# Optimization experiments

Measured on AMD Instinct MI355X. Metric: run time of the kernel, lower is better.

Reference implementation:

```python
import jax, jax.numpy as jnp
import numpy as np

B, N, E, H = 2, 2048, 1024, 16
D = E // H  # head_dim = 64


def setup_inputs() -> dict:
    key = jax.random.key(0)
    ks = jax.random.split(key, 8)
    s = 1.0 / np.sqrt(D)
    return {
        "query": jax.random.normal(ks[0], (B, N, E), jnp.float32),
        "key": jax.random.normal(ks[1], (B, N, E), jnp.float32),
        "value": jax.random.normal(ks[2], (B, N, E), jnp.float32),
        "mask": jax.random.randint(ks[3], (B, N), 0, 2, jnp.int32),
        # per-head Linear weights, torch layout (out_features, in_features) stacked over heads
        "Wq": jax.random.uniform(ks[4], (H, D, D), jnp.float32, -s, s),
        "Wk": jax.random.uniform(ks[5], (H, D, D), jnp.float32, -s, s),
        "Wv": jax.random.uniform(ks[6], (H, D, D), jnp.float32, -s, s),
        "Wo": jax.random.uniform(ks[7], (E, E), jnp.float32, -1.0 / np.sqrt(E), 1.0 / np.sqrt(E)),
    }


def reference(query, key, value, mask, Wq, Wk, Wv, Wo):
    b, n, e = query.shape
    h, d, _ = Wq.shape
    q = query.reshape(b, n, h, d)
    k = key.reshape(b, n, h, d)
    v = value.reshape(b, n, h, d)
    # per-head Linear (no bias): x @ W[i].T, batched over heads
    qh = jnp.einsum('bnhd,hed->bnhe', q, Wq)
    kh = jnp.einsum('bnhd,hed->bnhe', k, Wk)
    vh = jnp.einsum('bnhd,hed->bnhe', v, Wv)
    # NOTE: original scales by sqrt(embed_size), not sqrt(head_dim)
    scores = jnp.einsum('bqhd,bkhd->bhqk', qh, kh) / (e ** 0.5)
    # NOTE: mask is unsqueezed on the KEY axis position in torch (dim=2),
    # so it masks entire QUERY rows, broadcasting over keys.
    scores = jnp.where(mask[:, None, :, None] == 0, jnp.float32(-1e28), scores)
    probs = jax.nn.softmax(scores, axis=-1)
    attn = jnp.einsum('bhqk,bkhd->bqhd', probs, vh).reshape(b, n, e)
    return attn @ Wo.T
```

## Files before the change

### kernel.cpp

```cpp
#include <hip/hip_runtime.h>
#include <hip/hip_bf16.h>

#define B_ 2
#define N_ 2048
#define E_ 1024
#define H_ 16
#define D_ 64
#define BH_ (B_ * H_)

typedef __attribute__((ext_vector_type(4))) float f32x4;
typedef __attribute__((ext_vector_type(8))) short bf16x8;
typedef __attribute__((ext_vector_type(4))) short s16x4;
typedef __attribute__((ext_vector_type(4))) int i32x4;
typedef __attribute__((ext_vector_type(2))) int i32x2;
typedef __attribute__((ext_vector_type(4))) _Float16 f16x4;

#define MFMA(a, b, c) __builtin_amdgcn_mfma_f32_16x16x32_bf16(a, b, c, 0, 0, 0)
#define MFMA16(a, b, c) __builtin_amdgcn_mfma_f32_16x16x16f16(a, b, c, 0, 0, 0)

#define AS1(p) ((const __attribute__((address_space(1))) unsigned int*)(p))
#define AS3(p) ((__attribute__((address_space(3))) unsigned int*)(p))

static __device__ __forceinline__ int pack2bf(float lo, float hi) {
    __hip_bfloat162 t = __float22bfloat162_rn(float2{lo, hi});
    int r;
    __builtin_memcpy(&r, &t, 4);
    return r;
}
static __device__ __forceinline__ bf16x8 cvt8s(const float* __restrict__ p, float sc) {
    f32x4 a = *(const f32x4*)p;
    f32x4 b = *(const f32x4*)(p + 4);
    i32x4 r = {pack2bf(a.x * sc, a.y * sc), pack2bf(a.z * sc, a.w * sc),
               pack2bf(b.x * sc, b.y * sc), pack2bf(b.z * sc, b.w * sc)};
    return __builtin_bit_cast(bf16x8, r);
}
static __device__ __forceinline__ f16x4 pack4f16(f32x4 p) {
    auto lo = __builtin_amdgcn_cvt_pkrtz(p.x, p.y);
    auto hi = __builtin_amdgcn_cvt_pkrtz(p.z, p.w);
    f16x4 r;
    __builtin_memcpy(&r, &lo, 4);
    __builtin_memcpy(((char*)&r) + 4, &hi, 4);
    return r;
}

__global__ __launch_bounds__(256, 2)
void proj_kernel(const float* __restrict__ q, const float* __restrict__ k,
                 const float* __restrict__ v,
                 const float* __restrict__ Wq, const float* __restrict__ Wk,
                 const float* __restrict__ Wv,
                 const int* __restrict__ mask,
                 const float* __restrict__ Wo,
                 unsigned short* __restrict__ qh, unsigned short* __restrict__ kh,
                 unsigned short* __restrict__ vt, unsigned short* __restrict__ wob) {
    const int z = blockIdx.z;
    if (z == 3) {
        int idx = (blockIdx.y * 32 + blockIdx.x) * 256 + threadIdx.x;
        f32x4 w = *(const f32x4*)(Wo + (size_t)idx * 4);
        i32x2 r = {pack2bf(w.x, w.y), pack2bf(w.z, w.w)};
        *(i32x2*)(wob + (size_t)idx * 4) = r;
        return;
    }
    const float* X = (z == 0) ? q : (z == 1) ? k : v;
    const float* W = (z == 0) ? Wq : (z == 1) ? Wk : Wv;
    unsigned short* out = (z == 0) ? qh : (z == 1) ? kh : vt;
    const float wscale = (z == 0) ? (1.44269504f * 0.03125f) : 1.0f;

    const int lane = threadIdx.x & 63;
    const int wave = threadIdx.x >> 6;
    const int l16  = lane & 15;
    const int quad = lane >> 4;
    const int bh = blockIdx.y;
    const int b = bh >> 4, h = bh & 15;
    const int n0 = blockIdx.x * 64;
    const int tok = n0 + wave * 16 + l16;

    const float* xrow = X + ((size_t)(b * N_ + tok)) * E_ + h * 64;
    bf16x8 xf[2];
    xf[0] = cvt8s(xrow + quad * 8, 1.0f);
    xf[1] = cvt8s(xrow + 32 + quad * 8, 1.0f);

    const float* Wh = W + (size_t)h * 64 * 64;
    bf16x8 wf[4][2];
#pragma unroll
    for (int t4 = 0; t4 < 4; ++t4) {
        const float* wrow = Wh + (t4 * 16 + l16) * 64;
        wf[t4][0] = cvt8s(wrow + quad * 8, wscale);
        wf[t4][1] = cvt8s(wrow + 32 + quad * 8, wscale);
    }

    const int mk = (z == 0) ? mask[b * N_ + tok] : 1;

#pragma unroll
    for (int mi = 0; mi < 4; ++mi) {
        f32x4 a = {0.f, 0.f, 0.f, 0.f};
        a = MFMA(wf[mi][0], xf[0], a);
        a = MFMA(wf[mi][1], xf[1], a);
        if (z != 2) {
            i32x2 pk = {pack2bf(a.x, a.y), pack2bf(a.z, a.w)};
            if (!mk) pk = (i32x2){0, 0};
            *(i32x2*)(out + ((size_t)bh * N_ + tok) * 64 + mi * 16 + quad * 4) = pk;
        } else {
#pragma unroll
            for (int r = 0; r < 4; ++r) {
                int dout = mi * 16 + quad * 4 + r;
                _Float16 hv = (_Float16)a[r];
                unsigned short us;
                __builtin_memcpy(&us, &hv, 2);
                out[((size_t)bh * 64 + dout) * N_ + tok] = us;
            }
        }
    }
}

__global__ __launch_bounds__(256)
void cvt_wo_kernel(const float* __restrict__ wo, unsigned short* __restrict__ wob) {
    int idx = blockIdx.x * 256 + threadIdx.x;
    f32x4 v = *(const f32x4*)(wo + (size_t)idx * 4);
    i32x2 r = {pack2bf(v.x, v.y), pack2bf(v.z, v.w)};
    *(i32x2*)(wob + (size_t)idx * 4) = r;
}

__global__ __launch_bounds__(256, 2)
void attn_kernel(const unsigned short* __restrict__ qh,
                 const unsigned short* __restrict__ kh,
                 const unsigned short* __restrict__ vt,
                 unsigned short* __restrict__ attnb) {
    __shared__ short Kb[2][64 * 72];
    __shared__ short Vb[3][64 * 76];

    const int tid  = threadIdx.x;
    const int lane = tid & 63;
    const int wave = tid >> 6;
    const int l16  = lane & 15;
    const int quad = lane >> 4;

    const int flat = blockIdx.y * gridDim.x + blockIdx.x;
    const int qblk = flat >> 5;
    const int rem  = flat & 31;
    const int bh   = ((rem & 7) << 2) | (rem >> 3);
    const int b = bh >> 4, h = bh & 15;
    const int q0 = qblk * 128 + wave * 32;

    const unsigned short* kbase = kh + (size_t)bh * N_ * 64;
    const unsigned short* vbase = vt + (size_t)bh * 64 * N_;

    const int c0i = tid;
    const int c1i = tid + 256;
    const int k0o = (c0i >> 3) * 72 + (c0i & 7) * 8;
    const int k1o = (c1i >> 3) * 72 + (c1i & 7) * 8;
    const int v0o = (c0i >> 3) * 76 + (c0i & 7) * 8;
    const int v1o = (c1i >> 3) * 76 + (c1i & 7) * 8;

    short* kcur  = &Kb[0][0];
    short* knext = &Kb[1][0];
    short* vprev = &Vb[2][0];
    short* vcur  = &Vb[0][0];
    short* vnext = &Vb[1][0];

    bf16x8 qf[2][2];
#pragma unroll
    for (int qi = 0; qi < 2; ++qi) {
        const unsigned short* qrow = qh + ((size_t)bh * N_ + q0 + qi * 16 + l16) * 64;
        qf[qi][0] = *(const bf16x8*)(qrow + quad * 8);
        qf[qi][1] = *(const bf16x8*)(qrow + 32 + quad * 8);
    }

    f32x4 psum[2] = {{0.f, 0.f, 0.f, 0.f}, {0.f, 0.f, 0.f, 0.f}};
    f32x4 o[4][2];
#pragma unroll
    for (int mi = 0; mi < 4; ++mi)
#pragma unroll
        for (int qi = 0; qi < 2; ++qi) o[mi][qi] = (f32x4){0.f, 0.f, 0.f, 0.f};

    f16x4 pf[2][4];

    bf16x8 gK0, gK1, gV0, gV1;
    gK0 = *(const bf16x8*)(kbase + c0i * 8);
    gK1 = *(const bf16x8*)(kbase + c1i * 8);
    gV0 = *(const bf16x8*)(vbase + (size_t)(c0i >> 3) * N_ + (c0i & 7) * 8);
    gV1 = *(const bf16x8*)(vbase + (size_t)(c1i >> 3) * N_ + (c1i & 7) * 8);
    *(bf16x8*)(kcur + k0o) = gK0;
    *(bf16x8*)(kcur + k1o) = gK1;
    *(bf16x8*)(vcur + v0o) = gV0;
    *(bf16x8*)(vcur + v1o) = gV1;
    __syncthreads();

    for (int kt = 0; kt < N_ / 64; ++kt) {
        if (kt + 1 < N_ / 64) {
            const int k0n = (kt + 1) * 64;
            gK0 = *(const bf16x8*)(kbase + (size_t)k0n * 64 + c0i * 8);
            gK1 = *(const bf16x8*)(kbase + (size_t)k0n * 64 + c1i * 8);
            gV0 = *(const bf16x8*)(vbase + (size_t)(c0i >> 3) * N_ + k0n + (c0i & 7) * 8);
            gV1 = *(const bf16x8*)(vbase + (size_t)(c1i >> 3) * N_ + k0n + (c1i & 7) * 8);
        }

        __builtin_amdgcn_s_setprio(1);
        bf16x8 ka[4][2];
#pragma unroll
        for (int t4 = 0; t4 < 4; ++t4) {
            ka[t4][0] = *(const bf16x8*)(kcur + (t4 * 16 + l16) * 72 + quad * 8);
            ka[t4][1] = *(const bf16x8*)(kcur + (t4 * 16 + l16) * 72 + 32 + quad * 8);
        }
        f32x4 s[2][4];
#pragma unroll
        for (int qi = 0; qi < 2; ++qi)
#pragma unroll
            for (int t4 = 0; t4 < 4; ++t4) {
                f32x4 z = {0.f, 0.f, 0.f, 0.f};
                z = MFMA(ka[t4][0], qf[qi][0], z);
                z = MFMA(ka[t4][1], qf[qi][1], z);
                s[qi][t4] = z;
            }

        if (kt > 0) {
#pragma unroll
            for (int mi = 0; mi < 4; ++mi) {
#pragma unroll
                for (int t4 = 0; t4 < 4; ++t4) {
                    f16x4 va = *(const f16x4*)(vprev + (mi * 16 + l16) * 76 +
                                               t4 * 16 + quad * 4);
#pragma unroll
                    for (int qi = 0; qi < 2; ++qi)
                        o[mi][qi] = MFMA16(va, pf[qi][t4], o[mi][qi]);
                }
            }
        }
        __builtin_amdgcn_s_setprio(0);

#pragma unroll
        for (int qi = 0; qi < 2; ++qi) {
#pragma unroll
            for (int t4 = 0; t4 < 4; ++t4) {
                f32x4 p;
#pragma unroll
                for (int r = 0; r < 4; ++r) p[r] = __builtin_amdgcn_exp2f(s[qi][t4][r]);
                psum[qi] += p;
                pf[qi][t4] = pack4f16(p);
            }
        }

        if (kt + 1 < N_ / 64) {
            *(bf16x8*)(knext + k0o) = gK0;
            *(bf16x8*)(knext + k1o) = gK1;
            *(bf16x8*)(vnext + v0o) = gV0;
            *(bf16x8*)(vnext + v1o) = gV1;
            __syncthreads();
        }

        short* t = kcur; kcur = knext; knext = t;
        short* tv = vprev; vprev = vcur; vcur = vnext; vnext = tv;
    }

    __builtin_amdgcn_s_setprio(1);
#pragma unroll
    for (int mi = 0; mi < 4; ++mi) {
#pragma unroll
        for (int t4 = 0; t4 < 4; ++t4) {
            f16x4 va = *(const f16x4*)(vprev + (mi * 16 + l16) * 76 +
                                       t4 * 16 + quad * 4);
#pragma unroll
            for (int qi = 0; qi < 2; ++qi)
                o[mi][qi] = MFMA16(va, pf[qi][t4], o[mi][qi]);
        }
    }
    __builtin_amdgcn_s_setprio(0);

#pragma unroll
    for (int qi = 0; qi < 2; ++qi) {
        float rs = psum[qi].x + psum[qi].y + psum[qi].z + psum[qi].w;
        rs += __shfl_xor(rs, 16);
        rs += __shfl_xor(rs, 32);
        const float inv = 1.0f / rs;
        const int qrow_idx = q0 + qi * 16 + l16;
#pragma unroll
        for (int mi = 0; mi < 4; ++mi) {
            f32x4 ov = o[mi][qi];
            i32x2 pkk = {pack2bf(ov.x * inv, ov.y * inv),
                         pack2bf(ov.z * inv, ov.w * inv)};
            int d0 = mi * 16 + quad * 4;
            *(i32x2*)(attnb + ((size_t)(b * N_ + qrow_idx)) * E_ + h * 64 + d0) = pkk;
        }
    }
}

__global__ __launch_bounds__(512, 1)
void out_gemm_kernel(const unsigned short* __restrict__ A,
                     const unsigned short* __restrict__ Bw,
                     float* __restrict__ out) {
    __shared__ short As[2][128 * 32];
    __shared__ short Bs[2][128 * 32];

    const int tid  = threadIdx.x;
    const int lane = tid & 63;
    const int l16  = lane & 15;
    const int quad = lane >> 4;
    const int wave = tid >> 6;
    const int wm = wave & 1, wn = wave >> 1;

    const int flat = blockIdx.x;
    const int xcd  = flat & 7;
    const int sub  = flat >> 3;
    const int m0 = (xcd * 4 + (sub >> 3)) * 128;
    const int n0 = (sub & 7) * 128;

    const unsigned short* gA = A + (size_t)m0 * E_;
    const unsigned short* gB = Bw + (size_t)n0 * E_;

    f32x4 acc[4][2];
#pragma unroll
    for (int mt = 0; mt < 4; ++mt)
#pragma unroll
        for (int nt = 0; nt < 2; ++nt) acc[mt][nt] = (f32x4){0.f, 0.f, 0.f, 0.f};

    const int cc = tid >> 7, rr = tid & 127;
#define OG_STAGE(buf, k0)                                                        \
    {                                                                            \
        __builtin_amdgcn_global_load_lds(AS1(gA + (size_t)rr * E_ + (k0) + cc * 8), \
                                         AS3(&As[buf][tid * 8]), 16, 0, 0);      \
        __builtin_amdgcn_global_load_lds(AS1(gB + (size_t)rr * E_ + (k0) + cc * 8), \
                                         AS3(&Bs[buf][tid * 8]), 16, 0, 0);      \
    }

    OG_STAGE(0, 0)
    __syncthreads();

    for (int kt = 0; kt < E_ / 32; ++kt) {
        const int cur = kt & 1;
        if (kt + 1 < E_ / 32) OG_STAGE(cur ^ 1, (kt + 1) * 32)

        bf16x8 af[4], bf[2];
#pragma unroll
        for (int mt = 0; mt < 4; ++mt)
            af[mt] = *(const bf16x8*)(&As[cur][(quad * 128 + wm * 64 + mt * 16 + l16) * 8]);
#pragma unroll
        for (int nt = 0; nt < 2; ++nt)
            bf[nt] = *(const bf16x8*)(&Bs[cur][(quad * 128 + wn * 32 + nt * 16 + l16) * 8]);

        __builtin_amdgcn_s_setprio(1);
#pragma unroll
        for (int mt = 0; mt < 4; ++mt)
#pragma unroll
            for (int nt = 0; nt < 2; ++nt)
                acc[mt][nt] = MFMA(af[mt], bf[nt], acc[mt][nt]);
        __builtin_amdgcn_s_setprio(0);

        __syncthreads();
    }

#pragma unroll
    for (int mt = 0; mt < 4; ++mt)
#pragma unroll
        for (int nt = 0; nt < 2; ++nt)
#pragma unroll
            for (int r = 0; r < 4; ++r)
                out[(size_t)(m0 + wm * 64 + mt * 16 + quad * 4 + r) * E_ +
                    n0 + wn * 32 + nt * 16 + l16] = acc[mt][nt][r];
#undef OG_STAGE
}

extern "C" void kernel_launch(void* const* d_in, const int* in_sizes, int n_in,
                              void* d_out, int out_size, void* d_ws, size_t ws_size,
                              hipStream_t stream) {
    const float* q    = (const float*)d_in[0];
    const float* k    = (const float*)d_in[1];
    const float* v    = (const float*)d_in[2];
    const int*   mask = (const int*)d_in[3];
    const float* Wq   = (const float*)d_in[4];
    const float* Wk   = (const float*)d_in[5];
    const float* Wv   = (const float*)d_in[6];
    const float* Wo   = (const float*)d_in[7];
    float* out = (float*)d_out;

    char* ws = (char*)d_ws;
    unsigned short* qh    = (unsigned short*)(ws);
    unsigned short* kh    = (unsigned short*)(ws + (size_t)8 * 1024 * 1024);
    unsigned short* vt    = (unsigned short*)(ws + (size_t)16 * 1024 * 1024);
    unsigned short* attnb = (unsigned short*)(ws + (size_t)24 * 1024 * 1024);

    const bool fused_wo = ws_size >= (size_t)34 * 1024 * 1024;
    unsigned short* wob = fused_wo ? (unsigned short*)(ws + (size_t)32 * 1024 * 1024)
                                   : (unsigned short*)(ws);

    dim3 blk(256);
    proj_kernel<<<dim3(N_ / 64, BH_, fused_wo ? 4 : 3), blk, 0, stream>>>(
        q, k, v, Wq, Wk, Wv, mask, Wo, qh, kh, vt, wob);
    attn_kernel<<<dim3(16, 32), blk, 0, stream>>>(qh, kh, vt, attnb);
    if (!fused_wo)
        cvt_wo_kernel<<<dim3(E_ * E_ / 1024), blk, 0, stream>>>(Wo, wob);
    out_gemm_kernel<<<dim3(256), dim3(512), 0, stream>>>(attnb, wob, out);
}
```

Measured before the change: 197.5 us.

## Load K and V fragments directly from global memory, dropping LDS staging

Removes the shared-memory double/triple buffers and __syncthreads in the attention loop. Each wave now loads its K and V MFMA fragments straight from global (L2/L1) into registers, with K prefetched one tile ahead via ping-pong register arrays and the loop unrolled by two. The goal is to cut LDS traffic and barrier stalls, at the cost of every wave redundantly fetching the same K/V tiles from cache, narrower uncoalesced V loads, and more register pressure. The PV MFMA is no longer software-pipelined one iteration behind.

```diff
diff --git a/kernel.cpp b/kernel.cpp
--- a/kernel.cpp
+++ b/kernel.cpp
@@ -125,9 +125,6 @@
                  const unsigned short* __restrict__ kh,
                  const unsigned short* __restrict__ vt,
                  unsigned short* __restrict__ attnb) {
-    __shared__ short Kb[2][64 * 72];
-    __shared__ short Vb[3][64 * 76];
-
     const int tid  = threadIdx.x;
     const int lane = tid & 63;
     const int wave = tid >> 6;
@@ -144,19 +141,6 @@
     const unsigned short* kbase = kh + (size_t)bh * N_ * 64;
     const unsigned short* vbase = vt + (size_t)bh * 64 * N_;
 
-    const int c0i = tid;
-    const int c1i = tid + 256;
-    const int k0o = (c0i >> 3) * 72 + (c0i & 7) * 8;
-    const int k1o = (c1i >> 3) * 72 + (c1i & 7) * 8;
-    const int v0o = (c0i >> 3) * 76 + (c0i & 7) * 8;
-    const int v1o = (c1i >> 3) * 76 + (c1i & 7) * 8;
-
-    short* kcur  = &Kb[0][0];
-    short* knext = &Kb[1][0];
-    short* vprev = &Vb[2][0];
-    short* vcur  = &Vb[0][0];
-    short* vnext = &Vb[1][0];
-
     bf16x8 qf[2][2];
 #pragma unroll
     for (int qi = 0; qi < 2; ++qi) {
@@ -172,98 +156,78 @@
 #pragma unroll
         for (int qi = 0; qi < 2; ++qi) o[mi][qi] = (f32x4){0.f, 0.f, 0.f, 0.f};
 
-    f16x4 pf[2][4];
-
-    bf16x8 gK0, gK1, gV0, gV1;
-    gK0 = *(const bf16x8*)(kbase + c0i * 8);
-    gK1 = *(const bf16x8*)(kbase + c1i * 8);
-    gV0 = *(const bf16x8*)(vbase + (size_t)(c0i >> 3) * N_ + (c0i & 7) * 8);
-    gV1 = *(const bf16x8*)(vbase + (size_t)(c1i >> 3) * N_ + (c1i & 7) * 8);
-    *(bf16x8*)(kcur + k0o) = gK0;
-    *(bf16x8*)(kcur + k1o) = gK1;
-    *(bf16x8*)(vcur + v0o) = gV0;
-    *(bf16x8*)(vcur + v1o) = gV1;
-    __syncthreads();
-
-    for (int kt = 0; kt < N_ / 64; ++kt) {
-        if (kt + 1 < N_ / 64) {
-            const int k0n = (kt + 1) * 64;
-            gK0 = *(const bf16x8*)(kbase + (size_t)k0n * 64 + c0i * 8);
-            gK1 = *(const bf16x8*)(kbase + (size_t)k0n * 64 + c1i * 8);
-            gV0 = *(const bf16x8*)(vbase + (size_t)(c0i >> 3) * N_ + k0n + (c0i & 7) * 8);
-            gV1 = *(const bf16x8*)(vbase + (size_t)(c1i >> 3) * N_ + k0n + (c1i & 7) * 8);
+    const int koff = l16 * 64 + quad * 8;
+    const unsigned short* vrow = vbase + (size_t)l16 * N_ + quad * 4;
+
+    bf16x8 kaA[4][2], kaB[4][2];
+    {
+        const unsigned short* kp = kbase + koff;
+#pragma unroll
+        for (int t4 = 0; t4 < 4; ++t4) {
+            kaA[t4][0] = *(const bf16x8*)(kp + t4 * 1024);
+            kaA[t4][1] = *(const bf16x8*)(kp + t4 * 1024 + 32);
         }
-
-        __builtin_amdgcn_s_setprio(1);
-        bf16x8 ka[4][2];
-#pragma unroll
-        for (int t4 = 0; t4 < 4; ++t4) {
-            ka[t4][0] = *(const bf16x8*)(kcur + (t4 * 16 + l16) * 72 + quad * 8);
-            ka[t4][1] = *(const bf16x8*)(kcur + (t4 * 16 + l16) * 72 + 32 + quad * 8);
-        }
-        f32x4 s[2][4];
-#pragma unroll
-        for (int qi = 0; qi < 2; ++qi)
-#pragma unroll
-            for (int t4 = 0; t4 < 4; ++t4) {
-                f32x4 z = {0.f, 0.f, 0.f, 0.f};
-                z = MFMA(ka[t4][0], qf[qi][0], z);
-                z = MFMA(ka[t4][1], qf[qi][1], z);
-                s[qi][t4] = z;
-            }
-
-        if (kt > 0) {
-#pragma unroll
-            for (int mi = 0; mi < 4; ++mi) {
-#pragma unroll
-                for (int t4 = 0; t4 < 4; ++t4) {
-                    f16x4 va = *(const f16x4*)(vprev + (mi * 16 + l16) * 76 +
-                                               t4 * 16 + quad * 4);
-#pragma unroll
-                    for (int qi = 0; qi < 2; ++qi)
-                        o[mi][qi] = MFMA16(va, pf[qi][t4], o[mi][qi]);
-                }
-            }
-        }
-        __builtin_amdgcn_s_setprio(0);
-
-#pragma unroll
-        for (int qi = 0; qi < 2; ++qi) {
-#pragma unroll
-            for (int t4 = 0; t4 < 4; ++t4) {
-                f32x4 p;
-#pragma unroll
-                for (int r = 0; r < 4; ++r) p[r] = __builtin_amdgcn_exp2f(s[qi][t4][r]);
-                psum[qi] += p;
-                pf[qi][t4] = pack4f16(p);
-            }
-        }
-
-        if (kt + 1 < N_ / 64) {
-            *(bf16x8*)(knext + k0o) = gK0;
-            *(bf16x8*)(knext + k1o) = gK1;
-            *(bf16x8*)(vnext + v0o) = gV0;
-            *(bf16x8*)(vnext + v1o) = gV1;
-            __syncthreads();
-        }
-
-        short* t = kcur; kcur = knext; knext = t;
-        short* tv = vprev; vprev = vcur; vcur = vnext; vnext = tv;
-    }
-
-    __builtin_amdgcn_s_setprio(1);
-#pragma unroll
-    for (int mi = 0; mi < 4; ++mi) {
-#pragma unroll
-        for (int t4 = 0; t4 < 4; ++t4) {
-            f16x4 va = *(const f16x4*)(vprev + (mi * 16 + l16) * 76 +
-                                       t4 * 16 + quad * 4);
-#pragma unroll
-            for (int qi = 0; qi < 2; ++qi)
-                o[mi][qi] = MFMA16(va, pf[qi][t4], o[mi][qi]);
-        }
-    }
-    __builtin_amdgcn_s_setprio(0);
+    }
+
+#define ATTN_BODY(KT, KA_CUR, KA_NXT)                                            \
+    {                                                                            \
+        const int ktn = ((KT) + 1 < N_ / 64) ? (KT) + 1 : (N_ / 64 - 1);         \
+        const unsigned short* kp = kbase + (size_t)ktn * 4096 + koff;            \
+        _Pragma("unroll")                                                        \
+        for (int t4 = 0; t4 < 4; ++t4) {                                         \
+            KA_NXT[t4][0] = *(const bf16x8*)(kp + t4 * 1024);                    \
+            KA_NXT[t4][1] = *(const bf16x8*)(kp + t4 * 1024 + 32);               \
+        }                                                                        \
+        f16x4 va[4][4];                                                          \
+        {                                                                        \
+            const unsigned short* vp = vrow + (KT) * 64;                         \
+            _Pragma("unroll")                                                    \
+            for (int mi = 0; mi < 4; ++mi)                                       \
+                _Pragma("unroll")                                                \
+                for (int t4 = 0; t4 < 4; ++t4)                                   \
+                    va[mi][t4] = *(const f16x4*)(vp + (size_t)mi * 16 * N_ +     \
+                                                 t4 * 16);                       \
+        }                                                                        \
+        __builtin_amdgcn_s_setprio(1);                                           \
+        f32x4 s[2][4];                                                           \
+        _Pragma("unroll")                                                        \
+        for (int qi = 0; qi < 2; ++qi)                                           \
+            _Pragma("unroll")                                                    \
+            for (int t4 = 0; t4 < 4; ++t4) {                                     \
+                f32x4 zz = {0.f, 0.f, 0.f, 0.f};                                 \
+                zz = MFMA(KA_CUR[t4][0], qf[qi][0], zz);                         \
+                zz = MFMA(KA_CUR[t4][1], qf[qi][1], zz);                         \
+                s[qi][t4] = zz;                                                  \
+            }                                                                    \
+        __builtin_amdgcn_s_setprio(0);                                           \
+        f16x4 pf[2][4];                                                          \
+        _Pragma("unroll")                                                        \
+        for (int qi = 0; qi < 2; ++qi)                                           \
+            _Pragma("unroll")                                                    \
+            for (int t4 = 0; t4 < 4; ++t4) {                                     \
+                f32x4 p;                                                         \
+                _Pragma("unroll")                                                \
+                for (int r = 0; r < 4; ++r)                                      \
+                    p[r] = __builtin_amdgcn_exp2f(s[qi][t4][r]);                 \
+                psum[qi] += p;                                                   \
+                pf[qi][t4] = pack4f16(p);                                        \
+            }                                                                    \
+        __builtin_amdgcn_s_setprio(1);                                           \
+        _Pragma("unroll")                                                        \
+        for (int mi = 0; mi < 4; ++mi)                                           \
+            _Pragma("unroll")                                                    \
+            for (int t4 = 0; t4 < 4; ++t4)                                       \
+                _Pragma("unroll")                                                \
+                for (int qi = 0; qi < 2; ++qi)                                   \
+                    o[mi][qi] = MFMA16(va[mi][t4], pf[qi][t4], o[mi][qi]);       \
+        __builtin_amdgcn_s_setprio(0);                                           \
+    }
+
+    for (int kt = 0; kt < N_ / 64; kt += 2) {
+        ATTN_BODY(kt, kaA, kaB)
+        ATTN_BODY(kt + 1, kaB, kaA)
+    }
+#undef ATTN_BODY
 
 #pragma unroll
     for (int qi = 0; qi < 2; ++qi) {
```

After: 325.1 us. +64.6%, slower.

## Widen attention KV tiles to 128 keys and drop software-pipelined PV stage

Applied to the files above, without the earlier changes.

The attention kernel now loads 128-key K/V tiles per barrier instead of 64, halving the number of __syncthreads and global-load rounds. It processes each tile in two 64-key halves and does the PV MFMA in the same half as QK, which removes the previous one-step lag (the vprev triple buffer). This cuts synchronisation and loop overhead but loses the overlap of exp with the prior PV MFMAs. LDS use grows (roughly 36KB to 54KB), which may pressure occupancy at 2 blocks per CU.

```diff
diff --git a/kernel.cpp b/kernel.cpp
--- a/kernel.cpp
+++ b/kernel.cpp
@@ -10,7 +10,6 @@
 
 typedef __attribute__((ext_vector_type(4))) float f32x4;
 typedef __attribute__((ext_vector_type(8))) short bf16x8;
-typedef __attribute__((ext_vector_type(4))) short s16x4;
 typedef __attribute__((ext_vector_type(4))) int i32x4;
 typedef __attribute__((ext_vector_type(2))) int i32x2;
 typedef __attribute__((ext_vector_type(4))) _Float16 f16x4;
@@ -125,14 +124,14 @@
                  const unsigned short* __restrict__ kh,
                  const unsigned short* __restrict__ vt,
                  unsigned short* __restrict__ attnb) {
-    __shared__ short Kb[2][64 * 72];
-    __shared__ short Vb[3][64 * 76];
+    __shared__ short Kb[2][128 * 72];
+    __shared__ short Vb[2][64 * 140];
 
     const int tid  = threadIdx.x;
     const int lane = tid & 63;
-    const int wave = tid >> 6;
     const int l16  = lane & 15;
     const int quad = lane >> 4;
+    const int wave = tid >> 6;
 
     const int flat = blockIdx.y * gridDim.x + blockIdx.x;
     const int qblk = flat >> 5;
@@ -144,16 +143,13 @@
     const unsigned short* kbase = kh + (size_t)bh * N_ * 64;
     const unsigned short* vbase = vt + (size_t)bh * 64 * N_;
 
-    const int c0i = tid;
-    const int c1i = tid + 256;
-    const int k0o = (c0i >> 3) * 72 + (c0i & 7) * 8;
-    const int k1o = (c1i >> 3) * 72 + (c1i & 7) * 8;
-    const int v0o = (c0i >> 3) * 76 + (c0i & 7) * 8;
-    const int v1o = (c1i >> 3) * 76 + (c1i & 7) * 8;
+    const int ko = (tid >> 3) * 72 + (tid & 7) * 8;
+    const int vo = (tid >> 4) * 140 + (tid & 15) * 8;
+    const int vd = tid >> 4;
+    const int vc = (tid & 15) * 8;
 
     short* kcur  = &Kb[0][0];
     short* knext = &Kb[1][0];
-    short* vprev = &Vb[2][0];
     short* vcur  = &Vb[0][0];
     short* vnext = &Vb[1][0];
 
@@ -172,98 +168,93 @@
 #pragma unroll
         for (int qi = 0; qi < 2; ++qi) o[mi][qi] = (f32x4){0.f, 0.f, 0.f, 0.f};
 
-    f16x4 pf[2][4];
-
-    bf16x8 gK0, gK1, gV0, gV1;
-    gK0 = *(const bf16x8*)(kbase + c0i * 8);
-    gK1 = *(const bf16x8*)(kbase + c1i * 8);
-    gV0 = *(const bf16x8*)(vbase + (size_t)(c0i >> 3) * N_ + (c0i & 7) * 8);
-    gV1 = *(const bf16x8*)(vbase + (size_t)(c1i >> 3) * N_ + (c1i & 7) * 8);
-    *(bf16x8*)(kcur + k0o) = gK0;
-    *(bf16x8*)(kcur + k1o) = gK1;
-    *(bf16x8*)(vcur + v0o) = gV0;
-    *(bf16x8*)(vcur + v1o) = gV1;
+    bf16x8 gK[4], gV[4];
+#pragma unroll
+    for (int j = 0; j < 4; ++j) {
+        gK[j] = *(const bf16x8*)(kbase + (size_t)(tid + j * 256) * 8);
+        gV[j] = *(const bf16x8*)(vbase + (size_t)(vd + j * 16) * N_ + vc);
+    }
+#pragma unroll
+    for (int j = 0; j < 4; ++j) {
+        *(bf16x8*)(kcur + ko + j * 2304) = gK[j];
+        *(bf16x8*)(vcur + vo + j * 2240) = gV[j];
+    }
     __syncthreads();
 
-    for (int kt = 0; kt < N_ / 64; ++kt) {
-        if (kt + 1 < N_ / 64) {
-            const int k0n = (kt + 1) * 64;
-            gK0 = *(const bf16x8*)(kbase + (size_t)k0n * 64 + c0i * 8);
-            gK1 = *(const bf16x8*)(kbase + (size_t)k0n * 64 + c1i * 8);
-            gV0 = *(const bf16x8*)(vbase + (size_t)(c0i >> 3) * N_ + k0n + (c0i & 7) * 8);
-            gV1 = *(const bf16x8*)(vbase + (size_t)(c1i >> 3) * N_ + k0n + (c1i & 7) * 8);
-        }
-
-        __builtin_amdgcn_s_setprio(1);
-        bf16x8 ka[4][2];
-#pragma unroll
-        for (int t4 = 0; t4 < 4; ++t4) {
-            ka[t4][0] = *(const bf16x8*)(kcur + (t4 * 16 + l16) * 72 + quad * 8);
-            ka[t4][1] = *(const bf16x8*)(kcur + (t4 * 16 + l16) * 72 + 32 + quad * 8);
-        }
-        f32x4 s[2][4];
-#pragma unroll
-        for (int qi = 0; qi < 2; ++qi)
+    const int NT2 = N_ / 128;
+    for (int T = 0; T < NT2; ++T) {
+        if (T + 1 < NT2) {
+#pragma unroll
+            for (int j = 0; j < 4; ++j) {
+                gK[j] = *(const bf16x8*)(kbase + (size_t)(T + 1) * 8192 +
+                                         (size_t)(tid + j * 256) * 8);
+                gV[j] = *(const bf16x8*)(vbase + (size_t)(vd + j * 16) * N_ +
+                                         (T + 1) * 128 + vc);
+            }
+        }
+
+#pragma unroll
+        for (int hh = 0; hh < 2; ++hh) {
+            __builtin_amdgcn_s_setprio(1);
+            bf16x8 ka[4][2];
 #pragma unroll
             for (int t4 = 0; t4 < 4; ++t4) {
-                f32x4 z = {0.f, 0.f, 0.f, 0.f};
-                z = MFMA(ka[t4][0], qf[qi][0], z);
-                z = MFMA(ka[t4][1], qf[qi][1], z);
-                s[qi][t4] = z;
-            }
-
-        if (kt > 0) {
+                const int row = hh * 64 + t4 * 16 + l16;
+                ka[t4][0] = *(const bf16x8*)(kcur + row * 72 + quad * 8);
+                ka[t4][1] = *(const bf16x8*)(kcur + row * 72 + 32 + quad * 8);
+            }
+            f32x4 s[2][4];
+#pragma unroll
+            for (int qi = 0; qi < 2; ++qi)
+#pragma unroll
+                for (int t4 = 0; t4 < 4; ++t4) {
+                    f32x4 z = {0.f, 0.f, 0.f, 0.f};
+                    z = MFMA(ka[t4][0], qf[qi][0], z);
+                    z = MFMA(ka[t4][1], qf[qi][1], z);
+                    s[qi][t4] = z;
+                }
+            __builtin_amdgcn_s_setprio(0);
+
+            f16x4 pf[2][4];
+#pragma unroll
+            for (int qi = 0; qi < 2; ++qi)
+#pragma unroll
+                for (int t4 = 0; t4 < 4; ++t4) {
+                    f32x4 p;
+#pragma unroll
+                    for (int r = 0; r < 4; ++r)
+                        p[r] = __builtin_amdgcn_exp2f(s[qi][t4][r]);
+                    psum[qi] += p;
+                    pf[qi][t4] = pack4f16(p);
+                }
+
+            __builtin_amdgcn_s_setprio(1);
 #pragma unroll
             for (int mi = 0; mi < 4; ++mi) {
 #pragma unroll
                 for (int t4 = 0; t4 < 4; ++t4) {
-                    f16x4 va = *(const f16x4*)(vprev + (mi * 16 + l16) * 76 +
-                                               t4 * 16 + quad * 4);
+                    f16x4 va = *(const f16x4*)(vcur + (mi * 16 + l16) * 140 +
+                                               hh * 64 + t4 * 16 + quad * 4);
 #pragma unroll
                     for (int qi = 0; qi < 2; ++qi)
                         o[mi][qi] = MFMA16(va, pf[qi][t4], o[mi][qi]);
                 }
             }
-        }
-        __builtin_amdgcn_s_setprio(0);
-
-#pragma unroll
-        for (int qi = 0; qi < 2; ++qi) {
-#pragma unroll
-            for (int t4 = 0; t4 < 4; ++t4) {
-                f32x4 p;
-#pragma unroll
-                for (int r = 0; r < 4; ++r) p[r] = __builtin_amdgcn_exp2f(s[qi][t4][r]);
-                psum[qi] += p;
-                pf[qi][t4] = pack4f16(p);
-            }
-        }
-
-        if (kt + 1 < N_ / 64) {
-            *(bf16x8*)(knext + k0o) = gK0;
-            *(bf16x8*)(knext + k1o) = gK1;
-            *(bf16x8*)(vnext + v0o) = gV0;
-            *(bf16x8*)(vnext + v1o) = gV1;
+            __builtin_amdgcn_s_setprio(0);
+        }
+
+        if (T + 1 < NT2) {
+#pragma unroll
+            for (int j = 0; j < 4; ++j) {
+                *(bf16x8*)(knext + ko + j * 2304) = gK[j];
+                *(bf16x8*)(vnext + vo + j * 2240) = gV[j];
+            }
             __syncthreads();
         }
 
         short* t = kcur; kcur = knext; knext = t;
-        short* tv = vprev; vprev = vcur; vcur = vnext; vnext = tv;
-    }
-
-    __builtin_amdgcn_s_setprio(1);
-#pragma unroll
-    for (int mi = 0; mi < 4; ++mi) {
-#pragma unroll
-        for (int t4 = 0; t4 < 4; ++t4) {
-            f16x4 va = *(const f16x4*)(vprev + (mi * 16 + l16) * 76 +
-                                       t4 * 16 + quad * 4);
-#pragma unroll
-            for (int qi = 0; qi < 2; ++qi)
-                o[mi][qi] = MFMA16(va, pf[qi][t4], o[mi][qi]);
-        }
-    }
-    __builtin_amdgcn_s_setprio(0);
+        short* tv = vcur; vcur = vnext; vnext = tv;
+    }
 
 #pragma unroll
     for (int qi = 0; qi < 2; ++qi) {
```

After: 200.6 us. No clear change (+1.6%).
